# Kernel optimization log

Measured on AMD Instinct MI355X. Metric: run time of the kernel, lower is better.

## Reference

```python
import jax, jax.numpy as jnp
import numpy as np

N_NODES = 50000
N_EDGES = 400000
IN_DIM = 128
HID_DIM = 128
OUT_DIM = 128


def setup_inputs() -> dict:
    key = jax.random.key(0)
    k_x, k_e, k_w1, k_b1, k_w2, k_b2 = jax.random.split(key, 6)
    x = jax.random.normal(k_x, (N_NODES, IN_DIM), dtype=jnp.float32)
    edge_index = jax.random.randint(k_e, (2, N_EDGES), 0, N_NODES, dtype=jnp.int64)
    # nn.Linear-style params: W is [out, in], kaiming-uniform-ish init
    lim1 = 1.0 / np.sqrt(IN_DIM)
    lim2 = 1.0 / np.sqrt(HID_DIM)
    W1 = jax.random.uniform(k_w1, (HID_DIM, IN_DIM), jnp.float32, -lim1, lim1)
    b1 = jax.random.uniform(k_b1, (HID_DIM,), jnp.float32, -lim1, lim1)
    W2 = jax.random.uniform(k_w2, (OUT_DIM, HID_DIM), jnp.float32, -lim2, lim2)
    b2 = jax.random.uniform(k_b2, (OUT_DIM,), jnp.float32, -lim2, lim2)
    return {"x": x, "edge_index": edge_index, "W1": W1, "b1": b1, "W2": W2, "b2": b2}


def reference(x, edge_index, W1, b1, W2, b2):
    # h = relu(fc1(x));  dropout in eval mode -> identity
    h = jax.nn.relu(x @ W1.T + b1)                      # [N, hid]
    src, dst = edge_index[0], edge_index[1]
    # gather messages from src, scatter-add (mean) into dst
    agg = jax.ops.segment_sum(h[src], dst, num_segments=N_NODES)      # [N, hid]
    deg = jax.ops.segment_sum(jnp.ones_like(dst, dtype=h.dtype), dst,
                              num_segments=N_NODES)                   # [N]
    deg = jnp.maximum(deg, 1.0)
    agg = agg / deg[:, None]
    # residual add + fc2
    return (agg + h) @ W2.T + b2                        # [N, out]
```

## Files before the change

### kernel.cpp

```cpp
#include <hip/hip_runtime.h>

#define N_NODES 50000
#define N_EDGES 400000
#define DIM 128
#define N_SCAN_BLK ((N_NODES + 255) / 256)
#define CNT_BLK ((N_EDGES + 2047) / 2048)
#define FC1_BLK ((N_NODES + 63) / 64)
#define AGG_BLK ((N_NODES + 31) / 32)
#define PADDED_E (N_EDGES + 3 * N_NODES)

typedef unsigned short u16;
typedef unsigned int   u32;
typedef __bf16 v8bf  __attribute__((ext_vector_type(8)));
typedef float  f32x4 __attribute__((ext_vector_type(4)));
typedef u16    u16x8 __attribute__((ext_vector_type(8)));

union BF8 { u16x8 u; v8bf b; };

__device__ __forceinline__ float bf2f(u16 u) {
    union { u32 i; float f; } v; v.i = ((u32)u) << 16; return v.f;
}
__device__ __forceinline__ u16 f2bf(float f) {
    union { float f; u32 i; } v; v.f = f; u32 u = v.i;
    return (u16)((u + 0x7FFFu + ((u >> 16) & 1u)) >> 16);
}

__global__ __launch_bounds__(256, 3) void count_cast_fc1_kernel(
    const int* __restrict__ esrc, const int* __restrict__ edst,
    int* __restrict__ counts, int* __restrict__ occ,
    const float* __restrict__ W2, u16* __restrict__ Wb2,
    const float* __restrict__ x, const float* __restrict__ W1,
    const float* __restrict__ b1, u16* __restrict__ h)
{
    __shared__ u16 xs[64 * 136];
    const int bid = blockIdx.x;

    if (bid < CNT_BLK) {
        int e0 = bid * 2048 + threadIdx.x * 8;
        if (e0 + 8 <= N_EDGES) {
            int4 da = *(const int4*)(edst + e0);
            int4 db = *(const int4*)(edst + e0 + 4);
            int4 oa, ob;
            oa.x = atomicAdd(&counts[da.x], 1);
            oa.y = atomicAdd(&counts[da.y], 1);
            oa.z = atomicAdd(&counts[da.z], 1);
            oa.w = atomicAdd(&counts[da.w], 1);
            ob.x = atomicAdd(&counts[db.x], 1);
            ob.y = atomicAdd(&counts[db.y], 1);
            ob.z = atomicAdd(&counts[db.z], 1);
            ob.w = atomicAdd(&counts[db.w], 1);
            *(int4*)(occ + e0)     = oa;
            *(int4*)(occ + e0 + 4) = ob;
        } else if (e0 < N_EDGES) {
            for (int j = 0; j < 8 && e0 + j < N_EDGES; ++j)
                occ[e0 + j] = atomicAdd(&counts[edst[e0 + j]], 1);
        }
        return;
    }
    if (bid < CNT_BLK + 64) {
        int i = (bid - CNT_BLK) * 256 + threadIdx.x;
        Wb2[i] = f2bf(W2[i]);
        return;
    }
    if (bid == CNT_BLK + 64) {
        if (threadIdx.x < 128)
            *(u32*)(h + (size_t)N_NODES * DIM + threadIdx.x * 2) = 0u;
        return;
    }

    const int t = threadIdx.x;
    const int wave = t >> 6, lane = t & 63, quad = lane >> 4, l15 = lane & 15;
    const int ch = wave >> 1, rh = wave & 1;
    const int row0 = (bid - (CNT_BLK + 65)) * 64;

    BF8 barr[4][4];
#pragma unroll
    for (int ct = 0; ct < 4; ++ct)
#pragma unroll
        for (int ks = 0; ks < 4; ++ks) {
            const float* wp = W1 + (size_t)(ch * 64 + ct * 16 + l15) * DIM
                                 + ks * 32 + quad * 8;
            float4 f0 = *(const float4*)wp;
            float4 f1 = *(const float4*)(wp + 4);
            u16x8 p;
            p[0] = f2bf(f0.x); p[1] = f2bf(f0.y); p[2] = f2bf(f0.z); p[3] = f2bf(f0.w);
            p[4] = f2bf(f1.x); p[5] = f2bf(f1.y); p[6] = f2bf(f1.z); p[7] = f2bf(f1.w);
            barr[ct][ks].u = p;
        }

    {
        int srow = t >> 2, k0 = (t & 3) * 32;
        int grow = row0 + srow; if (grow >= N_NODES) grow = N_NODES - 1;
        const float* xp = x + (size_t)grow * DIM + k0;
#pragma unroll
        for (int j = 0; j < 4; ++j) {
            float4 f0 = *(const float4*)(xp + j * 8);
            float4 f1 = *(const float4*)(xp + j * 8 + 4);
            u16x8 p;
            p[0] = f2bf(f0.x); p[1] = f2bf(f0.y); p[2] = f2bf(f0.z); p[3] = f2bf(f0.w);
            p[4] = f2bf(f1.x); p[5] = f2bf(f1.y); p[6] = f2bf(f1.z); p[7] = f2bf(f1.w);
            *(u16x8*)&xs[srow * 136 + k0 + j * 8] = p;
        }
    }

    f32x4 acc[2][4];
#pragma unroll
    for (int ct = 0; ct < 4; ++ct) {
        float bv = b1[ch * 64 + ct * 16 + l15];
        acc[0][ct] = (f32x4){bv, bv, bv, bv};
        acc[1][ct] = (f32x4){bv, bv, bv, bv};
    }
    __syncthreads();

#pragma unroll
    for (int ks = 0; ks < 4; ++ks) {
        BF8 a0, a1;
        a0.u = *(const u16x8*)&xs[(rh * 32 +  0 + l15) * 136 + ks * 32 + quad * 8];
        a1.u = *(const u16x8*)&xs[(rh * 32 + 16 + l15) * 136 + ks * 32 + quad * 8];
#pragma unroll
        for (int ct = 0; ct < 4; ++ct) {
            acc[0][ct] = __builtin_amdgcn_mfma_f32_16x16x32_bf16(
                a0.b, barr[ct][ks].b, acc[0][ct], 0, 0, 0);
            acc[1][ct] = __builtin_amdgcn_mfma_f32_16x16x32_bf16(
                a1.b, barr[ct][ks].b, acc[1][ct], 0, 0, 0);
        }
    }

#pragma unroll
    for (int rt = 0; rt < 2; ++rt)
#pragma unroll
        for (int i = 0; i < 4; ++i) {
            int row = row0 + rh * 32 + rt * 16 + quad * 4 + i;
            if (row < N_NODES) {
#pragma unroll
                for (int ct = 0; ct < 4; ++ct) {
                    int col = ch * 64 + ct * 16 + l15;
                    h[(size_t)row * DIM + col] = f2bf(fmaxf(acc[rt][ct][i], 0.f));
                }
            }
        }
}

__global__ __launch_bounds__(256) void scan_ticket_kernel(
    const int* __restrict__ counts, int* __restrict__ row_ptr,
    int* __restrict__ gcursor, int* __restrict__ esorted)
{
    __shared__ int tmp[256];
    __shared__ int sbase;
    const int t = threadIdx.x;
    const int i = blockIdx.x * 256 + t;
    int deg = (i < N_NODES) ? counts[i] : 0;
    int p = (deg + 3) & ~3;
    tmp[t] = p;
    __syncthreads();
#pragma unroll
    for (int ofs = 1; ofs < 256; ofs <<= 1) {
        int add = (t >= ofs) ? tmp[t - ofs] : 0;
        __syncthreads();
        tmp[t] += add;
        __syncthreads();
    }
    if (t == 255) sbase = atomicAdd(gcursor, tmp[255]);
    __syncthreads();
    if (i < N_NODES) {
        int r = sbase + tmp[t] - p;
        row_ptr[i] = r;
        for (int k = deg; k < p; ++k) esorted[r + k] = N_NODES;
    }
}

__global__ __launch_bounds__(256) void scatter_kernel(
    const int* __restrict__ esrc, const int* __restrict__ edst,
    const int* __restrict__ occ, const int* __restrict__ row_ptr,
    int* __restrict__ esorted)
{
    int e0 = blockIdx.x * 2048 + threadIdx.x * 8;
    if (e0 + 8 <= N_EDGES) {
        int4 sa = *(const int4*)(esrc + e0);
        int4 sb = *(const int4*)(esrc + e0 + 4);
        int4 da = *(const int4*)(edst + e0);
        int4 db = *(const int4*)(edst + e0 + 4);
        int4 oa = *(const int4*)(occ + e0);
        int4 ob = *(const int4*)(occ + e0 + 4);
        esorted[row_ptr[da.x] + oa.x] = sa.x;
        esorted[row_ptr[da.y] + oa.y] = sa.y;
        esorted[row_ptr[da.z] + oa.z] = sa.z;
        esorted[row_ptr[da.w] + oa.w] = sa.w;
        esorted[row_ptr[db.x] + ob.x] = sb.x;
        esorted[row_ptr[db.y] + ob.y] = sb.y;
        esorted[row_ptr[db.z] + ob.z] = sb.z;
        esorted[row_ptr[db.w] + ob.w] = sb.w;
    } else if (e0 < N_EDGES) {
        for (int j = 0; j < 8 && e0 + j < N_EDGES; ++j)
            esorted[row_ptr[edst[e0 + j]] + occ[e0 + j]] = esrc[e0 + j];
    }
}

__global__ __launch_bounds__(256, 6) void agg_fc2_kernel(
    const int* __restrict__ row_ptr, const int* __restrict__ counts,
    const int* __restrict__ esorted, const u16* __restrict__ h,
    const u16* __restrict__ Wb2, const float* __restrict__ b2,
    float* __restrict__ out)
{
    __shared__ u16 xs[32 * 136];
    const int t = threadIdx.x;
    const int wv = t >> 6, lane = t & 63, quad = lane >> 4, l15 = lane & 15;
    const int row0 = blockIdx.x * 32;

    {
        const int s0 = wv * 8 + quad * 2;
        const int n0 = row0 + s0;
        const int n1 = n0 + 1;
        const bool va = (n0 < N_NODES), vb = (n1 < N_NODES);
        int start0 = 0, deg0 = 0, start1 = 0, deg1 = 0;
        if (va) { start0 = row_ptr[n0]; deg0 = counts[n0]; }
        if (vb) { start1 = row_ptr[n1]; deg1 = counts[n1]; }
        const int plen0 = (deg0 + 3) & ~3;
        const int plen1 = (deg1 + 3) & ~3;

        u16x8 hres0 = (u16x8){0,0,0,0,0,0,0,0};
        u16x8 hres1 = (u16x8){0,0,0,0,0,0,0,0};
        if (va) hres0 = *(const u16x8*)(h + (size_t)n0 * DIM + l15 * 8);
        if (vb) hres1 = *(const u16x8*)(h + (size_t)n1 * DIM + l15 * 8);

        float a0[8], a1[8];
#pragma unroll
        for (int j = 0; j < 8; ++j) { a0[j] = 0.f; a1[j] = 0.f; }

        const int* ep0 = esorted + start0;
        const int* ep1 = esorted + start1;
        int k0 = 0, k1 = 0;

        while (k0 < plen0 && k1 < plen1) {
            int4 ia = *(const int4*)(ep0 + k0);
            int4 ib = *(const int4*)(ep1 + k1);
            u16x8 v0 = *(const u16x8*)(h + (size_t)ia.x * DIM + l15 * 8);
            u16x8 v1 = *(const u16x8*)(h + (size_t)ia.y * DIM + l15 * 8);
            u16x8 v2 = *(const u16x8*)(h + (size_t)ia.z * DIM + l15 * 8);
            u16x8 v3 = *(const u16x8*)(h + (size_t)ia.w * DIM + l15 * 8);
            u16x8 w0 = *(const u16x8*)(h + (size_t)ib.x * DIM + l15 * 8);
            u16x8 w1 = *(const u16x8*)(h + (size_t)ib.y * DIM + l15 * 8);
            u16x8 w2 = *(const u16x8*)(h + (size_t)ib.z * DIM + l15 * 8);
            u16x8 w3 = *(const u16x8*)(h + (size_t)ib.w * DIM + l15 * 8);
#pragma unroll
            for (int j = 0; j < 8; ++j) {
                a0[j] += bf2f(v0[j]); a0[j] += bf2f(v1[j]);
                a0[j] += bf2f(v2[j]); a0[j] += bf2f(v3[j]);
                a1[j] += bf2f(w0[j]); a1[j] += bf2f(w1[j]);
                a1[j] += bf2f(w2[j]); a1[j] += bf2f(w3[j]);
            }
            k0 += 4; k1 += 4;
        }
        while (k0 + 8 <= plen0) {
            int4 ia = *(const int4*)(ep0 + k0);
            int4 ib = *(const int4*)(ep0 + k0 + 4);
            u16x8 v0 = *(const u16x8*)(h + (size_t)ia.x * DIM + l15 * 8);
            u16x8 v1 = *(const u16x8*)(h + (size_t)ia.y * DIM + l15 * 8);
            u16x8 v2 = *(const u16x8*)(h + (size_t)ia.z * DIM + l15 * 8);
            u16x8 v3 = *(const u16x8*)(h + (size_t)ia.w * DIM + l15 * 8);
            u16x8 v4 = *(const u16x8*)(h + (size_t)ib.x * DIM + l15 * 8);
            u16x8 v5 = *(const u16x8*)(h + (size_t)ib.y * DIM + l15 * 8);
            u16x8 v6 = *(const u16x8*)(h + (size_t)ib.z * DIM + l15 * 8);
            u16x8 v7 = *(const u16x8*)(h + (size_t)ib.w * DIM + l15 * 8);
#pragma unroll
            for (int j = 0; j < 8; ++j) {
                a0[j] += bf2f(v0[j]); a0[j] += bf2f(v1[j]);
                a0[j] += bf2f(v2[j]); a0[j] += bf2f(v3[j]);
                a0[j] += bf2f(v4[j]); a0[j] += bf2f(v5[j]);
                a0[j] += bf2f(v6[j]); a0[j] += bf2f(v7[j]);
            }
            k0 += 8;
        }
        if (k0 < plen0) {
            int4 ia = *(const int4*)(ep0 + k0);
            u16x8 v0 = *(const u16x8*)(h + (size_t)ia.x * DIM + l15 * 8);
            u16x8 v1 = *(const u16x8*)(h + (size_t)ia.y * DIM + l15 * 8);
            u16x8 v2 = *(const u16x8*)(h + (size_t)ia.z * DIM + l15 * 8);
            u16x8 v3 = *(const u16x8*)(h + (size_t)ia.w * DIM + l15 * 8);
#pragma unroll
            for (int j = 0; j < 8; ++j) {
                a0[j] += bf2f(v0[j]); a0[j] += bf2f(v1[j]);
                a0[j] += bf2f(v2[j]); a0[j] += bf2f(v3[j]);
            }
        }
        while (k1 + 8 <= plen1) {
            int4 ia = *(const int4*)(ep1 + k1);
            int4 ib = *(const int4*)(ep1 + k1 + 4);
            u16x8 v0 = *(const u16x8*)(h + (size_t)ia.x * DIM + l15 * 8);
            u16x8 v1 = *(const u16x8*)(h + (size_t)ia.y * DIM + l15 * 8);
            u16x8 v2 = *(const u16x8*)(h + (size_t)ia.z * DIM + l15 * 8);
            u16x8 v3 = *(const u16x8*)(h + (size_t)ia.w * DIM + l15 * 8);
            u16x8 v4 = *(const u16x8*)(h + (size_t)ib.x * DIM + l15 * 8);
            u16x8 v5 = *(const u16x8*)(h + (size_t)ib.y * DIM + l15 * 8);
            u16x8 v6 = *(const u16x8*)(h + (size_t)ib.z * DIM + l15 * 8);
            u16x8 v7 = *(const u16x8*)(h + (size_t)ib.w * DIM + l15 * 8);
#pragma unroll
            for (int j = 0; j < 8; ++j) {
                a1[j] += bf2f(v0[j]); a1[j] += bf2f(v1[j]);
                a1[j] += bf2f(v2[j]); a1[j] += bf2f(v3[j]);
                a1[j] += bf2f(v4[j]); a1[j] += bf2f(v5[j]);
                a1[j] += bf2f(v6[j]); a1[j] += bf2f(v7[j]);
            }
            k1 += 8;
        }
        if (k1 < plen1) {
            int4 ia = *(const int4*)(ep1 + k1);
            u16x8 v0 = *(const u16x8*)(h + (size_t)ia.x * DIM + l15 * 8);
            u16x8 v1 = *(const u16x8*)(h + (size_t)ia.y * DIM + l15 * 8);
            u16x8 v2 = *(const u16x8*)(h + (size_t)ia.z * DIM + l15 * 8);
            u16x8 v3 = *(const u16x8*)(h + (size_t)ia.w * DIM + l15 * 8);
#pragma unroll
            for (int j = 0; j < 8; ++j) {
                a1[j] += bf2f(v0[j]); a1[j] += bf2f(v1[j]);
                a1[j] += bf2f(v2[j]); a1[j] += bf2f(v3[j]);
            }
        }

        float inv0 = (deg0 > 0) ? 1.f / (float)deg0 : 1.f;
        float inv1 = (deg1 > 0) ? 1.f / (float)deg1 : 1.f;
        u16x8 pk0, pk1;
#pragma unroll
        for (int j = 0; j < 8; ++j) {
            pk0[j] = f2bf(a0[j] * inv0 + bf2f(hres0[j]));
            pk1[j] = f2bf(a1[j] * inv1 + bf2f(hres1[j]));
        }
        *(u16x8*)&xs[s0 * 136 + l15 * 8]       = pk0;
        *(u16x8*)&xs[(s0 + 1) * 136 + l15 * 8] = pk1;
    }

    BF8 barr[2][4];
#pragma unroll
    for (int ct = 0; ct < 2; ++ct)
#pragma unroll
        for (int ks = 0; ks < 4; ++ks)
            barr[ct][ks].u = *(const u16x8*)(
                Wb2 + (size_t)(wv * 32 + ct * 16 + l15) * DIM + ks * 32 + quad * 8);

    f32x4 acc[2][2];
#pragma unroll
    for (int ct = 0; ct < 2; ++ct) {
        float bv = b2[wv * 32 + ct * 16 + l15];
        acc[0][ct] = (f32x4){bv, bv, bv, bv};
        acc[1][ct] = (f32x4){bv, bv, bv, bv};
    }
    __syncthreads();

#pragma unroll
    for (int ks = 0; ks < 4; ++ks) {
        BF8 A0, A1;
        A0.u = *(const u16x8*)&xs[( 0 + l15) * 136 + ks * 32 + quad * 8];
        A1.u = *(const u16x8*)&xs[(16 + l15) * 136 + ks * 32 + quad * 8];
#pragma unroll
        for (int ct = 0; ct < 2; ++ct) {
            acc[0][ct] = __builtin_amdgcn_mfma_f32_16x16x32_bf16(
                A0.b, barr[ct][ks].b, acc[0][ct], 0, 0, 0);
            acc[1][ct] = __builtin_amdgcn_mfma_f32_16x16x32_bf16(
                A1.b, barr[ct][ks].b, acc[1][ct], 0, 0, 0);
        }
    }

#pragma unroll
    for (int rt = 0; rt < 2; ++rt)
#pragma unroll
        for (int i = 0; i < 4; ++i) {
            int row = row0 + rt * 16 + quad * 4 + i;
            if (row < N_NODES) {
#pragma unroll
                for (int ct = 0; ct < 2; ++ct) {
                    int col = wv * 32 + ct * 16 + l15;
                    out[(size_t)row * DIM + col] = acc[rt][ct][i];
                }
            }
        }
}

extern "C" void kernel_launch(void* const* d_in, const int* in_sizes, int n_in,
                              void* d_out, int out_size, void* d_ws, size_t ws_size,
                              hipStream_t stream)
{
    const float* x  = (const float*)d_in[0];
    const int*   ei = (const int*)d_in[1];
    const float* W1 = (const float*)d_in[2];
    const float* b1 = (const float*)d_in[3];
    const float* W2 = (const float*)d_in[4];
    const float* b2 = (const float*)d_in[5];
    float* out = (float*)d_out;

    const int* esrc = ei;
    const int* edst = ei + N_EDGES;

    char* ws = (char*)d_ws;
    size_t off = 0;
    u16* h       = (u16*)(ws + off); off += (size_t)(N_NODES + 1) * DIM * 2;
    u16* Wb2     = (u16*)(ws + off); off += (size_t)DIM * DIM * 2;
    int* counts  = (int*)(ws + off); off += (size_t)N_NODES * 4;
    int* gcursor = (int*)(ws + off); off += 4;
    int* row_ptr = (int*)(ws + off); off += (size_t)N_NODES * 4;
    int* occ     = (int*)(ws + off); off += (size_t)N_EDGES * 4;
    int* esorted = (int*)(ws + off); off += (size_t)PADDED_E * 4;

    hipMemsetAsync(counts, 0, (size_t)(N_NODES + 1) * 4, stream);

    count_cast_fc1_kernel<<<CNT_BLK + 65 + FC1_BLK, 256, 0, stream>>>(
        esrc, edst, counts, occ, W2, Wb2, x, W1, b1, h);
    scan_ticket_kernel<<<N_SCAN_BLK, 256, 0, stream>>>(
        counts, row_ptr, gcursor, esorted);
    scatter_kernel<<<CNT_BLK, 256, 0, stream>>>(
        esrc, edst, occ, row_ptr, esorted);
    agg_fc2_kernel<<<AGG_BLK, 256, 0, stream>>>(
        row_ptr, counts, esorted, h, Wb2, b2, out);
}
```

Baseline: 157.2 us.

## Fuse scan and scatter via grid barrier; prefetch edge indices in aggregation loop

Merges the scan/ticket kernel and the scatter kernel into one launch. A global atomic counter acts as a grid-wide barrier, which works because both stages use the same number of blocks and all blocks can be resident at once. This removes one kernel launch and its inter-kernel gap, at the cost of a spin-wait that could deadlock if the blocks were not co-resident. The paired-node aggregation loop also software-pipelines its edge-index loads, fetching the next int4 of indices before accumulating the current rows so that index-load latency is hidden.

```diff
diff --git a/kernel.cpp b/kernel.cpp
--- a/kernel.cpp
+++ b/kernel.cpp
@@ -141,14 +141,17 @@
         }
 }
 
-__global__ __launch_bounds__(256) void scan_ticket_kernel(
+__global__ __launch_bounds__(256) void scan_scatter_kernel(
     const int* __restrict__ counts, int* __restrict__ row_ptr,
-    int* __restrict__ gcursor, int* __restrict__ esorted)
+    int* __restrict__ gcursor, int* __restrict__ donecnt,
+    const int* __restrict__ esrc, const int* __restrict__ edst,
+    const int* __restrict__ occ, int* __restrict__ esorted)
 {
     __shared__ int tmp[256];
     __shared__ int sbase;
     const int t = threadIdx.x;
     const int i = blockIdx.x * 256 + t;
+
     int deg = (i < N_NODES) ? counts[i] : 0;
     int p = (deg + 3) & ~3;
     tmp[t] = p;
@@ -167,14 +170,18 @@
         row_ptr[i] = r;
         for (int k = deg; k < p; ++k) esorted[r + k] = N_NODES;
     }
-}
-
-__global__ __launch_bounds__(256) void scatter_kernel(
-    const int* __restrict__ esrc, const int* __restrict__ edst,
-    const int* __restrict__ occ, const int* __restrict__ row_ptr,
-    int* __restrict__ esorted)
-{
-    int e0 = blockIdx.x * 2048 + threadIdx.x * 8;
+
+    __threadfence();
+    __syncthreads();
+    if (t == 0) {
+        atomicAdd(donecnt, 1);
+        while (atomicAdd(donecnt, 0) < N_SCAN_BLK)
+            __builtin_amdgcn_s_sleep(8);
+    }
+    __syncthreads();
+    __threadfence();
+
+    int e0 = blockIdx.x * 2048 + t * 8;
     if (e0 + 8 <= N_EDGES) {
         int4 sa = *(const int4*)(esrc + e0);
         int4 sb = *(const int4*)(esrc + e0 + 4);
@@ -231,25 +238,35 @@
         const int* ep1 = esorted + start1;
         int k0 = 0, k1 = 0;
 
-        while (k0 < plen0 && k1 < plen1) {
-            int4 ia = *(const int4*)(ep0 + k0);
-            int4 ib = *(const int4*)(ep1 + k1);
-            u16x8 v0 = *(const u16x8*)(h + (size_t)ia.x * DIM + l15 * 8);
-            u16x8 v1 = *(const u16x8*)(h + (size_t)ia.y * DIM + l15 * 8);
-            u16x8 v2 = *(const u16x8*)(h + (size_t)ia.z * DIM + l15 * 8);
-            u16x8 v3 = *(const u16x8*)(h + (size_t)ia.w * DIM + l15 * 8);
-            u16x8 w0 = *(const u16x8*)(h + (size_t)ib.x * DIM + l15 * 8);
-            u16x8 w1 = *(const u16x8*)(h + (size_t)ib.y * DIM + l15 * 8);
-            u16x8 w2 = *(const u16x8*)(h + (size_t)ib.z * DIM + l15 * 8);
-            u16x8 w3 = *(const u16x8*)(h + (size_t)ib.w * DIM + l15 * 8);
-#pragma unroll
-            for (int j = 0; j < 8; ++j) {
-                a0[j] += bf2f(v0[j]); a0[j] += bf2f(v1[j]);
-                a0[j] += bf2f(v2[j]); a0[j] += bf2f(v3[j]);
-                a1[j] += bf2f(w0[j]); a1[j] += bf2f(w1[j]);
-                a1[j] += bf2f(w2[j]); a1[j] += bf2f(w3[j]);
-            }
-            k0 += 4; k1 += 4;
+        if (k0 < plen0 && k1 < plen1) {
+            int4 ia = *(const int4*)(ep0);
+            int4 ib = *(const int4*)(ep1);
+            while (true) {
+                u16x8 v0 = *(const u16x8*)(h + (size_t)ia.x * DIM + l15 * 8);
+                u16x8 v1 = *(const u16x8*)(h + (size_t)ia.y * DIM + l15 * 8);
+                u16x8 v2 = *(const u16x8*)(h + (size_t)ia.z * DIM + l15 * 8);
+                u16x8 v3 = *(const u16x8*)(h + (size_t)ia.w * DIM + l15 * 8);
+                u16x8 w0 = *(const u16x8*)(h + (size_t)ib.x * DIM + l15 * 8);
+                u16x8 w1 = *(const u16x8*)(h + (size_t)ib.y * DIM + l15 * 8);
+                u16x8 w2 = *(const u16x8*)(h + (size_t)ib.z * DIM + l15 * 8);
+                u16x8 w3 = *(const u16x8*)(h + (size_t)ib.w * DIM + l15 * 8);
+                k0 += 4; k1 += 4;
+                const bool more = (k0 < plen0) & (k1 < plen1);
+                int4 ian, ibn;
+                if (more) {
+                    ian = *(const int4*)(ep0 + k0);
+                    ibn = *(const int4*)(ep1 + k1);
+                }
+#pragma unroll
+                for (int j = 0; j < 8; ++j) {
+                    a0[j] += bf2f(v0[j]); a0[j] += bf2f(v1[j]);
+                    a0[j] += bf2f(v2[j]); a0[j] += bf2f(v3[j]);
+                    a1[j] += bf2f(w0[j]); a1[j] += bf2f(w1[j]);
+                    a1[j] += bf2f(w2[j]); a1[j] += bf2f(w3[j]);
+                }
+                if (!more) break;
+                ia = ian; ib = ibn;
+            }
         }
         while (k0 + 8 <= plen0) {
             int4 ia = *(const int4*)(ep0 + k0);
@@ -395,18 +412,17 @@
     u16* Wb2     = (u16*)(ws + off); off += (size_t)DIM * DIM * 2;
     int* counts  = (int*)(ws + off); off += (size_t)N_NODES * 4;
     int* gcursor = (int*)(ws + off); off += 4;
+    int* donecnt = (int*)(ws + off); off += 4;
     int* row_ptr = (int*)(ws + off); off += (size_t)N_NODES * 4;
     int* occ     = (int*)(ws + off); off += (size_t)N_EDGES * 4;
     int* esorted = (int*)(ws + off); off += (size_t)PADDED_E * 4;
 
-    hipMemsetAsync(counts, 0, (size_t)(N_NODES + 1) * 4, stream);
+    hipMemsetAsync(counts, 0, (size_t)(N_NODES + 2) * 4, stream);
 
     count_cast_fc1_kernel<<<CNT_BLK + 65 + FC1_BLK, 256, 0, stream>>>(
         esrc, edst, counts, occ, W2, Wb2, x, W1, b1, h);
-    scan_ticket_kernel<<<N_SCAN_BLK, 256, 0, stream>>>(
-        counts, row_ptr, gcursor, esorted);
-    scatter_kernel<<<CNT_BLK, 256, 0, stream>>>(
-        esrc, edst, occ, row_ptr, esorted);
+    scan_scatter_kernel<<<N_SCAN_BLK, 256, 0, stream>>>(
+        counts, row_ptr, gcursor, donecnt, esrc, edst, occ, esorted);
     agg_fc2_kernel<<<AGG_BLK, 256, 0, stream>>>(
         row_ptr, counts, esorted, h, Wb2, b2, out);
 }
```

Result: slower. 198.3 us (+26.2%).
